# Performance work log

Hardware: AMD Instinct MI355X
Metric: run time of the kernel (lower is better)

## Reference

```python
import jax, jax.numpy as jnp
import numpy as np

EPS_D = 1e-05
EPS_LOG = 1e-05
H_BAND = 0.5


def setup_inputs() -> dict:
    key = jax.random.key(0)
    k1, k2 = jax.random.split(key)
    N, C, Hh, Ww = 4, 256, 64, 64
    y = jax.random.normal(k1, (N, C, Hh, Ww), dtype=jnp.float32)
    y_hat = jax.random.normal(k2, (N, C, Hh, Ww), dtype=jnp.float32)
    return {"y": y, "y_hat": y_hat}


def contextual_loss(x, y, h=H_BAND):
    # x, y: (N, C, H, W)
    N, C, Hh, Ww = x.shape
    # mean over W, H, N of y -> per-channel mu, broadcast as (1, C, 1, 1)
    y_mu = y.mean(axis=3).mean(axis=2).mean(axis=0).reshape(1, C, 1, 1)
    x_c = x - y_mu
    y_c = y - y_mu
    x_n = x_c / jnp.linalg.norm(x_c, ord=2, axis=1, keepdims=True)
    y_n = y_c / jnp.linalg.norm(y_c, ord=2, axis=1, keepdims=True)
    x_n = x_n.reshape(N, C, Hh * Ww)  # (N, C, P)
    y_n = y_n.reshape(N, C, Hh * Ww)
    # cosine similarity: (N, P, P)
    cosine_sim = jnp.einsum('ncp,ncq->npq', x_n, y_n)
    d = 1.0 - cosine_sim
    d_min = jnp.min(d, axis=2, keepdims=True)
    d_tilde = d / (d_min + EPS_D)
    w = jnp.exp((1.0 - d_tilde) / h)
    cx_ij = w / jnp.sum(w, axis=2, keepdims=True)
    cx = jnp.mean(jnp.max(cx_ij, axis=1), axis=1)  # (N,)
    return jnp.mean(-jnp.log(cx + EPS_LOG))


def reference(y, y_hat):
    return contextual_loss(y, y_hat)
```

## Files before the change

### kernel.cpp

```cpp
#include <hip/hip_runtime.h>
#include <hip/hip_bf16.h>
#include <math.h>


namespace {
constexpr int NB = 4;
constexpr int C  = 256;
constexpr int P  = 4096;
constexpr float EPSD = 1e-5f;
constexpr float EPSL = 1e-5f;
constexpr float HB   = 0.5f;

constexpr size_t OFF_MU    = 0;
constexpr size_t OFF_XNT   = 256;
constexpr size_t OFF_YNT   = OFF_XNT + (size_t)NB * P * C / 2;
constexpr size_t OFF_XS    = OFF_YNT + (size_t)NB * P * C / 2;
constexpr size_t OFF_RMAXH = OFF_XS + (size_t)NB * P * C / 2;
constexpr size_t OFF_SUMH  = OFF_RMAXH + (size_t)NB * 2 * P;
constexpr size_t OFF_CMAXH = OFF_SUMH + (size_t)NB * 2 * P;
constexpr size_t OFF_RMAX  = OFF_CMAXH + (size_t)NB * 2 * P;
constexpr size_t OFF_ALPHA = OFF_RMAX + (size_t)NB * P;
constexpr size_t OFF_LROW  = OFF_ALPHA + (size_t)NB * P;
}

typedef __attribute__((ext_vector_type(8))) __bf16 bf16x8;
typedef __attribute__((ext_vector_type(16))) float f32x16;
typedef unsigned short u16;

__device__ __forceinline__ bf16x8 ldfrag(const u16* p) {
  return *reinterpret_cast<const bf16x8*>(p);
}
__device__ __forceinline__ void gload_lds16(const u16* g, u16* l) {
  __builtin_amdgcn_global_load_lds(
      (const __attribute__((address_space(1))) void*)g,
      (__attribute__((address_space(3))) void*)l, 16, 0, 0);
}
__device__ __forceinline__ f32x16 zero16() {
  f32x16 z;
#pragma unroll
  for (int i = 0; i < 16; ++i) z[i] = 0.f;
  return z;
}

__device__ __forceinline__ void stage_tile64(const u16* __restrict__ src, int row0,
                                             u16* lds, int t) {
#pragma unroll
  for (int i = 0; i < 8; ++i) {
    const int g  = i * 256 + t;
    const int r  = g >> 5;
    const int gs = (g & 31) ^ (r & 15);
    gload_lds16(src + (size_t)(row0 + r) * 256 + gs * 8, lds + (size_t)g * 8);
  }
}

__global__ void k_mu(const float* __restrict__ yh, float* __restrict__ ws) {
  const int c = blockIdx.x;
  const int t = threadIdx.x;
  float s = 0.f;
  for (int n = 0; n < NB; ++n) {
    const float* base = yh + ((size_t)(n * C + c)) * P;
    for (int p = t; p < P; p += 256) s += base[p];
  }
  __shared__ float red[256];
  red[t] = s;
  __syncthreads();
  for (int w = 128; w > 0; w >>= 1) {
    if (t < w) red[t] += red[t + w];
    __syncthreads();
  }
  if (t == 0) ws[OFF_MU + c] = red[0] * (1.0f / (NB * P));
}

__global__ __launch_bounds__(256) void k_norm(const float* __restrict__ x,
                                              const float* __restrict__ yh,
                                              float* __restrict__ ws) {
  const int b     = blockIdx.x;
  const int arr   = b & 1;
  const int strip = (b >> 1) & 63;
  const int n     = b >> 7;
  const int t     = threadIdx.x;
  const int w     = t >> 6;
  const int l     = t & 63;

  __shared__ float mu_s[C];
  __shared__ float tile[64][257];
  __shared__ float red[4][64];
  __shared__ float invs[64];

  mu_s[t] = ws[OFF_MU + t];
  __syncthreads();

  const float* src = arr ? yh : x;
  const size_t base = ((size_t)n * C) * P + (size_t)strip * 64 + l;
  float ssq = 0.f;
  for (int cc = 0; cc < C; cc += 4) {
    const int c = cc + w;
    const float v = src[base + (size_t)c * P] - mu_s[c];
    tile[l][c] = v;
    ssq += v * v;
  }
  red[w][l] = ssq;
  __syncthreads();
  if (t < 64) invs[t] = 1.0f / sqrtf(red[0][t] + red[1][t] + red[2][t] + red[3][t]);
  __syncthreads();

  uint* dst = reinterpret_cast<uint*>(ws + (arr ? OFF_YNT : OFF_XNT));
  const int c2 = t & 127;
  const size_t drow = ((size_t)n * P + (size_t)strip * 64) * (C / 2);
  for (int it = 0; it < 32; ++it) {
    const int pl = it * 2 + (t >> 7);
    const float s  = invs[pl];
    const float v0 = tile[pl][2 * c2] * s;
    const float v1 = tile[pl][2 * c2 + 1] * s;
    const unsigned short u0 = __builtin_bit_cast(unsigned short, __float2bfloat16(v0));
    const unsigned short u1 = __builtin_bit_cast(unsigned short, __float2bfloat16(v1));
    dst[drow + (size_t)pl * (C / 2) + c2] = ((uint)u1 << 16) | u0;
  }
}

template <int PASS>
__global__ __launch_bounds__(256, 1) void k_rows(float* __restrict__ ws) {
  const int t = threadIdx.x;
  const int wave = t >> 6, l = t & 63, l31 = l & 31, lh = l >> 5, l15 = l31 & 15;
  const int rt = wave >> 1, ct = wave & 1;
  const int bid = blockIdx.x;
  const int qh = bid & 1, n = (bid >> 1) & 3, strip = bid >> 3;
  const int p0 = strip * 128;
  const int qbase = qh * 2048;

  const u16* A = reinterpret_cast<const u16*>(ws + (PASS == 0 ? OFF_XNT : OFF_XS)) +
                 (size_t)n * P * C;
  const u16* yn = reinterpret_cast<const u16*>(ws + OFF_YNT) + (size_t)n * P * C;

  __shared__ __align__(16) u16 Bl[3][64 * 256];
  __shared__ float red[4][64];

  const u16* Ap0 = A + (size_t)(p0 + rt * 64 + l31) * 256;
  bf16x8 af0[16], af1[16];
#pragma unroll
  for (int ks = 0; ks < 16; ++ks) {
    af0[ks] = ldfrag(Ap0 + (ks * 2 + lh) * 8);
    af1[ks] = ldfrag(Ap0 + 32 * 256 + (ks * 2 + lh) * 8);
  }

  float run0[16], run1[16];
#pragma unroll
  for (int r = 0; r < 16; ++r) {
    run0[r] = (PASS == 0) ? -3.0e38f : 0.f;
    run1[r] = (PASS == 0) ? -3.0e38f : 0.f;
  }

  stage_tile64(yn, qbase, Bl[0], t);
  stage_tile64(yn, qbase + 64, Bl[1], t);

  int cur = 0;
  for (int step = 0; step < 32; ++step) {
    if (step < 31) {
      asm volatile("s_waitcnt vmcnt(8)" ::: "memory");
    } else {
      asm volatile("s_waitcnt vmcnt(0)" ::: "memory");
    }
    __builtin_amdgcn_sched_barrier(0);
    __builtin_amdgcn_s_barrier();
    __builtin_amdgcn_sched_barrier(0);
    if (step + 2 < 32) {
      const int nb = (cur == 0) ? 2 : cur - 1;
      stage_tile64(yn, qbase + (step + 2) * 64, Bl[nb], t);
    }

    const u16* Brow = &Bl[cur][(size_t)(ct * 32 + l31) * 256];
    f32x16 a0 = zero16(), a1 = zero16();
#pragma unroll
    for (int ks = 0; ks < 16; ++ks) {
      const bf16x8 bq = ldfrag(Brow + ((ks * 2 + lh) ^ l15) * 8);
      a0 = __builtin_amdgcn_mfma_f32_32x32x16_bf16(af0[ks], bq, a0, 0, 0, 0);
      a1 = __builtin_amdgcn_mfma_f32_32x32x16_bf16(af1[ks], bq, a1, 0, 0, 0);
    }

    if (PASS == 0) {
#pragma unroll
      for (int r = 0; r < 16; ++r) {
        run0[r] = fmaxf(run0[r], a0[r]);
        run1[r] = fmaxf(run1[r], a1[r]);
      }
    } else {
#pragma unroll
      for (int r = 0; r < 16; ++r) {
        run0[r] += __expf(a0[r]);
        run1[r] += __expf(a1[r]);
      }
    }
    cur = (cur == 2) ? 0 : cur + 1;
  }

#pragma unroll
  for (int m = 1; m <= 16; m <<= 1) {
#pragma unroll
    for (int r = 0; r < 16; ++r) {
      const float o0 = __shfl_xor(run0[r], m, 64);
      const float o1 = __shfl_xor(run1[r], m, 64);
      run0[r] = (PASS == 0) ? fmaxf(run0[r], o0) : (run0[r] + o0);
      run1[r] = (PASS == 0) ? fmaxf(run1[r], o1) : (run1[r] + o1);
    }
  }
  if (l31 == 0) {
#pragma unroll
    for (int r = 0; r < 16; ++r) {
      const int row = (r & 3) + 8 * (r >> 2) + 4 * lh;
      red[wave][row]      = run0[r];
      red[wave][row + 32] = run1[r];
    }
  }
  __syncthreads();
  if (t < 128) {
    const int rt2 = t >> 6, row = t & 63;
    const float v0 = red[rt2 * 2][row], v1 = red[rt2 * 2 + 1][row];
    const size_t o = (size_t)(n * 2 + qh) * P + p0 + rt2 * 64 + row;
    if (PASS == 0)
      ws[OFF_RMAXH + o] = fmaxf(v0, v1);
    else
      ws[OFF_SUMH + o] = v0 + v1;
  }
}

__global__ void k_alpha(float* __restrict__ ws) {
  const int i = blockIdx.x * 256 + threadIdx.x;
  const int n = i >> 12, p = i & (P - 1);
  const float rm = fmaxf(ws[OFF_RMAXH + (size_t)(n * 2) * P + p],
                         ws[OFF_RMAXH + (size_t)(n * 2 + 1) * P + p]);
  ws[OFF_RMAX + (size_t)n * P + p]  = rm;
  ws[OFF_ALPHA + (size_t)n * P + p] = 1.0f / (HB * (1.0f - rm + EPSD));
}

__global__ __launch_bounds__(256) void k_scale(float* __restrict__ ws) {
  const int g = blockIdx.x * 256 + threadIdx.x;
  const int rowg = g >> 5;
  const int n = rowg >> 12, p = rowg & (P - 1);
  const float a = ws[OFF_ALPHA + (size_t)n * P + p];
  const uint4 v = reinterpret_cast<const uint4*>(ws + OFF_XNT)[g];
  uint4 o;
  uint* vi = (uint*)&v;
  uint* oi = (uint*)&o;
#pragma unroll
  for (int j = 0; j < 4; ++j) {
    const uint u = vi[j];
    const float f0 = __builtin_bit_cast(float, (u & 0xffffu) << 16) * a;
    const float f1 = __builtin_bit_cast(float, (u & 0xffff0000u)) * a;
    const unsigned short b0 = __builtin_bit_cast(unsigned short, __float2bfloat16(f0));
    const unsigned short b1 = __builtin_bit_cast(unsigned short, __float2bfloat16(f1));
    oi[j] = ((uint)b1 << 16) | b0;
  }
  reinterpret_cast<uint4*>(ws + OFF_XS)[g] = o;
}

__global__ void k_L(float* __restrict__ ws) {
  const int i = blockIdx.x * 256 + threadIdx.x;
  const int n = i >> 12, p = i & (P - 1);
  const float s = ws[OFF_SUMH + (size_t)(n * 2) * P + p] +
                  ws[OFF_SUMH + (size_t)(n * 2 + 1) * P + p];
  ws[OFF_LROW + (size_t)n * P + p] = logf(s);
}

__global__ __launch_bounds__(256, 1) void k_colp(float* __restrict__ ws) {
  const int t = threadIdx.x;
  const int wave = t >> 6, l = t & 63, l31 = l & 31, lh = l >> 5, l15 = l31 & 15;
  const int rt = wave >> 1, ct = wave & 1;
  const int bid = blockIdx.x;
  const int ph = bid & 1, n = (bid >> 1) & 3, qstrip = bid >> 3;
  const int q0 = qstrip * 128;
  const int pbase = ph * 2048;

  const u16* yn = reinterpret_cast<const u16*>(ws + OFF_YNT) + (size_t)n * P * C;
  const u16* xs = reinterpret_cast<const u16*>(ws + OFF_XS) + (size_t)n * P * C;
  const float* lrw = ws + OFF_LROW + (size_t)n * P;

  __shared__ __align__(16) u16 Bl[3][64 * 256];
  __shared__ float red[4][64];
  __shared__ float Lsh[2048];

  const u16* Ap0 = yn + (size_t)(q0 + rt * 64 + l31) * 256;
  bf16x8 af0[16], af1[16];
#pragma unroll
  for (int ks = 0; ks < 16; ++ks) {
    af0[ks] = ldfrag(Ap0 + (ks * 2 + lh) * 8);
    af1[ks] = ldfrag(Ap0 + 32 * 256 + (ks * 2 + lh) * 8);
  }

  for (int i = t; i < 2048; i += 256) Lsh[i] = lrw[pbase + i];
  __syncthreads();

  float run0[16], run1[16];
#pragma unroll
  for (int r = 0; r < 16; ++r) { run0[r] = -3.0e38f; run1[r] = -3.0e38f; }

  stage_tile64(xs, pbase, Bl[0], t);
  stage_tile64(xs, pbase + 64, Bl[1], t);

  int cur = 0;
  for (int step = 0; step < 32; ++step) {
    if (step < 31) {
      asm volatile("s_waitcnt vmcnt(8)" ::: "memory");
    } else {
      asm volatile("s_waitcnt vmcnt(0)" ::: "memory");
    }
    __builtin_amdgcn_sched_barrier(0);
    __builtin_amdgcn_s_barrier();
    __builtin_amdgcn_sched_barrier(0);
    if (step + 2 < 32) {
      const int nb = (cur == 0) ? 2 : cur - 1;
      stage_tile64(xs, pbase + (step + 2) * 64, Bl[nb], t);
    }

    const float L_ = Lsh[step * 64 + ct * 32 + l31];

    const u16* Brow = &Bl[cur][(size_t)(ct * 32 + l31) * 256];
    f32x16 a0 = zero16(), a1 = zero16();
#pragma unroll
    for (int ks = 0; ks < 16; ++ks) {
      const bf16x8 bq = ldfrag(Brow + ((ks * 2 + lh) ^ l15) * 8);
      a0 = __builtin_amdgcn_mfma_f32_32x32x16_bf16(af0[ks], bq, a0, 0, 0, 0);
      a1 = __builtin_amdgcn_mfma_f32_32x32x16_bf16(af1[ks], bq, a1, 0, 0, 0);
    }
#pragma unroll
    for (int r = 0; r < 16; ++r) {
      run0[r] = fmaxf(run0[r], a0[r] - L_);
      run1[r] = fmaxf(run1[r], a1[r] - L_);
    }
    cur = (cur == 2) ? 0 : cur + 1;
  }

#pragma unroll
  for (int m = 1; m <= 16; m <<= 1) {
#pragma unroll
    for (int r = 0; r < 16; ++r) {
      run0[r] = fmaxf(run0[r], __shfl_xor(run0[r], m, 64));
      run1[r] = fmaxf(run1[r], __shfl_xor(run1[r], m, 64));
    }
  }
  if (l31 == 0) {
#pragma unroll
    for (int r = 0; r < 16; ++r) {
      const int row = (r & 3) + 8 * (r >> 2) + 4 * lh;
      red[wave][row]      = run0[r];
      red[wave][row + 32] = run1[r];
    }
  }
  __syncthreads();
  if (t < 128) {
    const int rt2 = t >> 6, row = t & 63;
    const float v = fmaxf(red[rt2 * 2][row], red[rt2 * 2 + 1][row]);
    ws[OFF_CMAXH + (size_t)(n * 2 + ph) * P + q0 + rt2 * 64 + row] = v;
  }
}

__global__ void k_final(const float* __restrict__ ws, float* __restrict__ out) {
  const int t = threadIdx.x;
  __shared__ float red[256];
  __shared__ float lsum_s;
  if (t == 0) lsum_s = 0.f;
  for (int n = 0; n < NB; ++n) {
    float e = 0.f;
    for (int q = t; q < P; q += 256) {
      const float m = fmaxf(ws[OFF_CMAXH + (size_t)(n * 2) * P + q],
                            ws[OFF_CMAXH + (size_t)(n * 2 + 1) * P + q]);
      e += __expf(m);
    }
    __syncthreads();
    red[t] = e;
    __syncthreads();
    for (int w = 128; w > 0; w >>= 1) {
      if (t < w) red[t] += red[t + w];
      __syncthreads();
    }
    if (t == 0) lsum_s += -logf(red[0] * (1.0f / P) + EPSL);
  }
  __syncthreads();
  if (t == 0) out[0] = lsum_s * 0.25f;
}

extern "C" void kernel_launch(void* const* d_in, const int* in_sizes, int n_in,
                              void* d_out, int out_size, void* d_ws, size_t ws_size,
                              hipStream_t stream) {
  const float* x  = (const float*)d_in[0];
  const float* yh = (const float*)d_in[1];
  float* ws  = (float*)d_ws;
  float* out = (float*)d_out;

  k_mu<<<dim3(C), dim3(256), 0, stream>>>(yh, ws);
  k_norm<<<dim3(NB * 64 * 2), dim3(256), 0, stream>>>(x, yh, ws);
  k_rows<0><<<dim3(256), dim3(256), 0, stream>>>(ws);
  k_alpha<<<dim3(NB * P / 256), dim3(256), 0, stream>>>(ws);
  k_scale<<<dim3(NB * P * C / 8 / 256), dim3(256), 0, stream>>>(ws);
  k_rows<1><<<dim3(256), dim3(256), 0, stream>>>(ws);
  k_L<<<dim3(NB * P / 256), dim3(256), 0, stream>>>(ws);
  k_colp<<<dim3(256), dim3(256), 0, stream>>>(ws);
  k_final<<<dim3(1), dim3(256), 0, stream>>>(ws, out);
}
```

Measured before the change: 216.3 us.

## Split column range into quarters, double-buffer LDS, and raise MFMA priority

The three GEMM-style kernels now split the inner dimension into four 1024-wide parts instead of two, doubling the grid to 512 blocks. This gives better occupancy across the 256 CUs. Staging drops from triple to double buffering with an extra barrier per step, the reduction scratch reuses the tile buffer, and k_colp keeps its log-sum values in registers instead of LDS. s_setprio is raised around the MFMA loops. Partial results grow to four per row, so the follow-up reduction kernels read more data, and the added barrier lowers overlap within each block.

```diff
diff --git a/kernel.cpp b/kernel.cpp
--- a/kernel.cpp
+++ b/kernel.cpp
@@ -16,9 +16,9 @@
 constexpr size_t OFF_YNT   = OFF_XNT + (size_t)NB * P * C / 2;
 constexpr size_t OFF_XS    = OFF_YNT + (size_t)NB * P * C / 2;
 constexpr size_t OFF_RMAXH = OFF_XS + (size_t)NB * P * C / 2;
-constexpr size_t OFF_SUMH  = OFF_RMAXH + (size_t)NB * 2 * P;
-constexpr size_t OFF_CMAXH = OFF_SUMH + (size_t)NB * 2 * P;
-constexpr size_t OFF_RMAX  = OFF_CMAXH + (size_t)NB * 2 * P;
+constexpr size_t OFF_SUMH  = OFF_RMAXH + (size_t)NB * 4 * P;
+constexpr size_t OFF_CMAXH = OFF_SUMH + (size_t)NB * 4 * P;
+constexpr size_t OFF_RMAX  = OFF_CMAXH + (size_t)NB * 4 * P;
 constexpr size_t OFF_ALPHA = OFF_RMAX + (size_t)NB * P;
 constexpr size_t OFF_LROW  = OFF_ALPHA + (size_t)NB * P;
 }
@@ -124,16 +124,15 @@
   const int wave = t >> 6, l = t & 63, l31 = l & 31, lh = l >> 5, l15 = l31 & 15;
   const int rt = wave >> 1, ct = wave & 1;
   const int bid = blockIdx.x;
-  const int qh = bid & 1, n = (bid >> 1) & 3, strip = bid >> 3;
+  const int qp = bid & 3, n = (bid >> 2) & 3, strip = bid >> 4;
   const int p0 = strip * 128;
-  const int qbase = qh * 2048;
+  const int qbase = qp * 1024;
 
   const u16* A = reinterpret_cast<const u16*>(ws + (PASS == 0 ? OFF_XNT : OFF_XS)) +
                  (size_t)n * P * C;
   const u16* yn = reinterpret_cast<const u16*>(ws + OFF_YNT) + (size_t)n * P * C;
 
-  __shared__ __align__(16) u16 Bl[3][64 * 256];
-  __shared__ float red[4][64];
+  __shared__ __align__(16) u16 Bl[2][64 * 256];
 
   const u16* Ap0 = A + (size_t)(p0 + rt * 64 + l31) * 256;
   bf16x8 af0[16], af1[16];
@@ -142,6 +141,8 @@
     af0[ks] = ldfrag(Ap0 + (ks * 2 + lh) * 8);
     af1[ks] = ldfrag(Ap0 + 32 * 256 + (ks * 2 + lh) * 8);
   }
+  asm volatile("s_waitcnt vmcnt(0)" ::: "memory");
+  __builtin_amdgcn_sched_barrier(0);
 
   float run0[16], run1[16];
 #pragma unroll
@@ -151,11 +152,10 @@
   }
 
   stage_tile64(yn, qbase, Bl[0], t);
-  stage_tile64(yn, qbase + 64, Bl[1], t);
-
-  int cur = 0;
-  for (int step = 0; step < 32; ++step) {
-    if (step < 31) {
+
+  for (int step = 0; step < 16; ++step) {
+    if (step + 1 < 16) {
+      stage_tile64(yn, qbase + (step + 1) * 64, Bl[(step + 1) & 1], t);
       asm volatile("s_waitcnt vmcnt(8)" ::: "memory");
     } else {
       asm volatile("s_waitcnt vmcnt(0)" ::: "memory");
@@ -163,19 +163,17 @@
     __builtin_amdgcn_sched_barrier(0);
     __builtin_amdgcn_s_barrier();
     __builtin_amdgcn_sched_barrier(0);
-    if (step + 2 < 32) {
-      const int nb = (cur == 0) ? 2 : cur - 1;
-      stage_tile64(yn, qbase + (step + 2) * 64, Bl[nb], t);
-    }
-
-    const u16* Brow = &Bl[cur][(size_t)(ct * 32 + l31) * 256];
+
+    const u16* Brow = &Bl[step & 1][(size_t)(ct * 32 + l31) * 256];
     f32x16 a0 = zero16(), a1 = zero16();
+    __builtin_amdgcn_s_setprio(1);
 #pragma unroll
     for (int ks = 0; ks < 16; ++ks) {
       const bf16x8 bq = ldfrag(Brow + ((ks * 2 + lh) ^ l15) * 8);
       a0 = __builtin_amdgcn_mfma_f32_32x32x16_bf16(af0[ks], bq, a0, 0, 0, 0);
       a1 = __builtin_amdgcn_mfma_f32_32x32x16_bf16(af1[ks], bq, a1, 0, 0, 0);
     }
+    __builtin_amdgcn_s_setprio(0);
 
     if (PASS == 0) {
 #pragma unroll
@@ -190,7 +188,8 @@
         run1[r] += __expf(a1[r]);
       }
     }
-    cur = (cur == 2) ? 0 : cur + 1;
+    __builtin_amdgcn_sched_barrier(0);
+    __builtin_amdgcn_s_barrier();
   }
 
 #pragma unroll
@@ -203,6 +202,7 @@
       run1[r] = (PASS == 0) ? fmaxf(run1[r], o1) : (run1[r] + o1);
     }
   }
+  float (*red)[64] = reinterpret_cast<float(*)[64]>(&Bl[0][0]);
   if (l31 == 0) {
 #pragma unroll
     for (int r = 0; r < 16; ++r) {
@@ -215,7 +215,7 @@
   if (t < 128) {
     const int rt2 = t >> 6, row = t & 63;
     const float v0 = red[rt2 * 2][row], v1 = red[rt2 * 2 + 1][row];
-    const size_t o = (size_t)(n * 2 + qh) * P + p0 + rt2 * 64 + row;
+    const size_t o = (size_t)(n * 4 + qp) * P + p0 + rt2 * 64 + row;
     if (PASS == 0)
       ws[OFF_RMAXH + o] = fmaxf(v0, v1);
     else
@@ -226,8 +226,10 @@
 __global__ void k_alpha(float* __restrict__ ws) {
   const int i = blockIdx.x * 256 + threadIdx.x;
   const int n = i >> 12, p = i & (P - 1);
-  const float rm = fmaxf(ws[OFF_RMAXH + (size_t)(n * 2) * P + p],
-                         ws[OFF_RMAXH + (size_t)(n * 2 + 1) * P + p]);
+  float rm = ws[OFF_RMAXH + (size_t)(n * 4) * P + p];
+#pragma unroll
+  for (int j = 1; j < 4; ++j)
+    rm = fmaxf(rm, ws[OFF_RMAXH + (size_t)(n * 4 + j) * P + p]);
   ws[OFF_RMAX + (size_t)n * P + p]  = rm;
   ws[OFF_ALPHA + (size_t)n * P + p] = 1.0f / (HB * (1.0f - rm + EPSD));
 }
@@ -256,8 +258,10 @@
 __global__ void k_L(float* __restrict__ ws) {
   const int i = blockIdx.x * 256 + threadIdx.x;
   const int n = i >> 12, p = i & (P - 1);
-  const float s = ws[OFF_SUMH + (size_t)(n * 2) * P + p] +
-                  ws[OFF_SUMH + (size_t)(n * 2 + 1) * P + p];
+  float s = 0.f;
+#pragma unroll
+  for (int j = 0; j < 4; ++j)
+    s += ws[OFF_SUMH + (size_t)(n * 4 + j) * P + p];
   ws[OFF_LROW + (size_t)n * P + p] = logf(s);
 }
 
@@ -266,17 +270,15 @@
   const int wave = t >> 6, l = t & 63, l31 = l & 31, lh = l >> 5, l15 = l31 & 15;
   const int rt = wave >> 1, ct = wave & 1;
   const int bid = blockIdx.x;
-  const int ph = bid & 1, n = (bid >> 1) & 3, qstrip = bid >> 3;
+  const int pp = bid & 3, n = (bid >> 2) & 3, qstrip = bid >> 4;
   const int q0 = qstrip * 128;
-  const int pbase = ph * 2048;
+  const int pbase = pp * 1024;
 
   const u16* yn = reinterpret_cast<const u16*>(ws + OFF_YNT) + (size_t)n * P * C;
   const u16* xs = reinterpret_cast<const u16*>(ws + OFF_XS) + (size_t)n * P * C;
   const float* lrw = ws + OFF_LROW + (size_t)n * P;
 
-  __shared__ __align__(16) u16 Bl[3][64 * 256];
-  __shared__ float red[4][64];
-  __shared__ float Lsh[2048];
+  __shared__ __align__(16) u16 Bl[2][64 * 256];
 
   const u16* Ap0 = yn + (size_t)(q0 + rt * 64 + l31) * 256;
   bf16x8 af0[16], af1[16];
@@ -285,20 +287,23 @@
     af0[ks] = ldfrag(Ap0 + (ks * 2 + lh) * 8);
     af1[ks] = ldfrag(Ap0 + 32 * 256 + (ks * 2 + lh) * 8);
   }
-
-  for (int i = t; i < 2048; i += 256) Lsh[i] = lrw[pbase + i];
-  __syncthreads();
+  float Lr[16];
+#pragma unroll
+  for (int s = 0; s < 16; ++s) Lr[s] = lrw[pbase + s * 64 + ct * 32 + l31];
+
+  asm volatile("s_waitcnt vmcnt(0)" ::: "memory");
+  __builtin_amdgcn_sched_barrier(0);
 
   float run0[16], run1[16];
 #pragma unroll
   for (int r = 0; r < 16; ++r) { run0[r] = -3.0e38f; run1[r] = -3.0e38f; }
 
   stage_tile64(xs, pbase, Bl[0], t);
-  stage_tile64(xs, pbase + 64, Bl[1], t);
-
-  int cur = 0;
-  for (int step = 0; step < 32; ++step) {
-    if (step < 31) {
+
+#pragma unroll
+  for (int step = 0; step < 16; ++step) {
+    if (step + 1 < 16) {
+      stage_tile64(xs, pbase + (step + 1) * 64, Bl[(step + 1) & 1], t);
       asm volatile("s_waitcnt vmcnt(8)" ::: "memory");
     } else {
       asm volatile("s_waitcnt vmcnt(0)" ::: "memory");
@@ -306,27 +311,26 @@
     __builtin_amdgcn_sched_barrier(0);
     __builtin_amdgcn_s_barrier();
     __builtin_amdgcn_sched_barrier(0);
-    if (step + 2 < 32) {
-      const int nb = (cur == 0) ? 2 : cur - 1;
-      stage_tile64(xs, pbase + (step + 2) * 64, Bl[nb], t);
-    }
-
-    const float L_ = Lsh[step * 64 + ct * 32 + l31];
-
-    const u16* Brow = &Bl[cur][(size_t)(ct * 32 + l31) * 256];
+
+    const float L_ = Lr[step];
+
+    const u16* Brow = &Bl[step & 1][(size_t)(ct * 32 + l31) * 256];
     f32x16 a0 = zero16(), a1 = zero16();
+    __builtin_amdgcn_s_setprio(1);
 #pragma unroll
     for (int ks = 0; ks < 16; ++ks) {
       const bf16x8 bq = ldfrag(Brow + ((ks * 2 + lh) ^ l15) * 8);
       a0 = __builtin_amdgcn_mfma_f32_32x32x16_bf16(af0[ks], bq, a0, 0, 0, 0);
       a1 = __builtin_amdgcn_mfma_f32_32x32x16_bf16(af1[ks], bq, a1, 0, 0, 0);
     }
+    __builtin_amdgcn_s_setprio(0);
 #pragma unroll
     for (int r = 0; r < 16; ++r) {
       run0[r] = fmaxf(run0[r], a0[r] - L_);
       run1[r] = fmaxf(run1[r], a1[r] - L_);
     }
-    cur = (cur == 2) ? 0 : cur + 1;
+    __builtin_amdgcn_sched_barrier(0);
+    __builtin_amdgcn_s_barrier();
   }
 
 #pragma unroll
@@ -337,6 +341,7 @@
       run1[r] = fmaxf(run1[r], __shfl_xor(run1[r], m, 64));
     }
   }
+  float (*red)[64] = reinterpret_cast<float(*)[64]>(&Bl[0][0]);
   if (l31 == 0) {
 #pragma unroll
     for (int r = 0; r < 16; ++r) {
@@ -349,7 +354,7 @@
   if (t < 128) {
     const int rt2 = t >> 6, row = t & 63;
     const float v = fmaxf(red[rt2 * 2][row], red[rt2 * 2 + 1][row]);
-    ws[OFF_CMAXH + (size_t)(n * 2 + ph) * P + q0 + rt2 * 64 + row] = v;
+    ws[OFF_CMAXH + (size_t)(n * 4 + pp) * P + q0 + rt2 * 64 + row] = v;
   }
 }
 
@@ -361,8 +366,10 @@
   for (int n = 0; n < NB; ++n) {
     float e = 0.f;
     for (int q = t; q < P; q += 256) {
-      const float m = fmaxf(ws[OFF_CMAXH + (size_t)(n * 2) * P + q],
-                            ws[OFF_CMAXH + (size_t)(n * 2 + 1) * P + q]);
+      float m = ws[OFF_CMAXH + (size_t)(n * 4) * P + q];
+#pragma unroll
+      for (int j = 1; j < 4; ++j)
+        m = fmaxf(m, ws[OFF_CMAXH + (size_t)(n * 4 + j) * P + q]);
       e += __expf(m);
     }
     __syncthreads();
@@ -388,11 +395,11 @@
 
   k_mu<<<dim3(C), dim3(256), 0, stream>>>(yh, ws);
   k_norm<<<dim3(NB * 64 * 2), dim3(256), 0, stream>>>(x, yh, ws);
-  k_rows<0><<<dim3(256), dim3(256), 0, stream>>>(ws);
+  k_rows<0><<<dim3(512), dim3(256), 0, stream>>>(ws);
   k_alpha<<<dim3(NB * P / 256), dim3(256), 0, stream>>>(ws);
   k_scale<<<dim3(NB * P * C / 8 / 256), dim3(256), 0, stream>>>(ws);
-  k_rows<1><<<dim3(256), dim3(256), 0, stream>>>(ws);
+  k_rows<1><<<dim3(512), dim3(256), 0, stream>>>(ws);
   k_L<<<dim3(NB * P / 256), dim3(256), 0, stream>>>(ws);
-  k_colp<<<dim3(256), dim3(256), 0, stream>>>(ws);
+  k_colp<<<dim3(512), dim3(256), 0, stream>>>(ws);
   k_final<<<dim3(1), dim3(256), 0, stream>>>(ws, out);
 }
```

New measurement: 206.8 us. 4.4% less time.
